# Performance work log

Measured on AMD Instinct MI355X. Metric: run time of the kernel, lower is better.

Reference implementation:

```python
import jax, jax.numpy as jnp
import numpy as np
from jax import lax

SQRT2 = float(np.sqrt(2.0))  # lrelu def_gain
LRELU_SLOPE = 0.2


def setup_inputs() -> dict:
    key = jax.random.key(0)
    ks = jax.random.split(key, 4)
    N, I, O, WD, H = 16, 256, 512, 512, 64
    return {
        "x": jax.random.normal(ks[0], (N, I, H, H), dtype=jnp.float32),
        "w": jax.random.normal(ks[1], (N, WD), dtype=jnp.float32),
        "affine_w": jax.random.normal(ks[2], (I, WD), dtype=jnp.float32),
        "affine_b": jnp.ones((I,), dtype=jnp.float32),
        "weight": jax.random.normal(ks[3], (O, I, 3, 3), dtype=jnp.float32),
        "bias": jnp.zeros((O,), dtype=jnp.float32),
    }


def reference(x, w, affine_w, affine_b, weight, bias):
    N, I, H, W = x.shape
    O, _, kh, kw = weight.shape
    w_dim = affine_w.shape[1]

    # affine (FullyConnectedLayer, weight_gain = 1/sqrt(w_dim))
    styles = w @ (affine_w.T / np.sqrt(w_dim)) + affine_b  # [N, I]

    # modulate + demodulate -> per-sample weights [N, O, I, kh, kw]
    ww = weight[None] * styles[:, None, :, None, None]
    dcoefs = lax.rsqrt(jnp.sum(ww * ww, axis=(2, 3, 4)) + 1e-8)  # [N, O]
    ww = ww * dcoefs[:, :, None, None, None]

    # resample filter: outer([1,3,3,1])/sum, symmetric so flip is a no-op
    f1 = jnp.array([1.0, 3.0, 3.0, 1.0], dtype=x.dtype)
    f1 = f1 / f1.sum()
    f2 = jnp.outer(f1, f1)  # [4, 4]

    # upfirdn2d: pad by padding + (fw-down+1)//2 = 2 per side, depthwise 4x4
    xp = jnp.pad(x, ((0, 0), (0, 0), (2, 2), (2, 2)))
    fk = jnp.broadcast_to(f2[None, None], (I, 1, 4, 4))
    xf = lax.conv_general_dilated(
        xp, fk, window_strides=(1, 1), padding="VALID",
        feature_group_count=I,
        dimension_numbers=("NCHW", "OIHW", "NCHW"))  # [N, I, H+1, W+1]

    # fused grouped conv, stride 2; flip_weight=False -> flip kernel spatially
    wk = ww[:, :, :, ::-1, ::-1].reshape(N * O, I, kh, kw)
    xg = xf.reshape(1, N * I, xf.shape[2], xf.shape[3])
    y = lax.conv_general_dilated(
        xg, wk, window_strides=(2, 2), padding="VALID",
        feature_group_count=N,
        dimension_numbers=("NCHW", "OIHW", "NCHW"))
    y = y.reshape(N, O, y.shape[2], y.shape[3])  # [N, O, H/2, W/2]

    # bias + lrelu, act_gain = sqrt(2), no clamp
    y = y + bias[None, :, None, None]
    y = jnp.where(y >= 0, y, LRELU_SLOPE * y) * SQRT2
    return y
```

## Files before the change

kernel.cpp:

```cpp
#include <hip/hip_runtime.h>
#include <cstdint>
#include <cstddef>


typedef short bf16x8 __attribute__((ext_vector_type(8)));
typedef float f32x4  __attribute__((ext_vector_type(4)));

#define CGSTR 4460544
#define NSTR  278784
#define PLSTR 69696

__device__ __forceinline__ unsigned short f2bf(float f) {
  union { float f; unsigned u; } v; v.f = f;
  unsigned r = (v.u + 0x7FFFu + ((v.u >> 16) & 1u)) >> 16;
  return (unsigned short)r;
}

__device__ __forceinline__ void gload_lds16(const void* g, void* l) {
  __builtin_amdgcn_global_load_lds((const __attribute__((address_space(1))) void*)g,
                                   (__attribute__((address_space(3))) void*)l,
                                   16, 0, 0);
}

__global__ void styles_kernel(const float* __restrict__ w, const float* __restrict__ aw,
                              const float* __restrict__ ab, float* __restrict__ styles) {
  const int n = blockIdx.x;
  const int i = threadIdx.x;
  const float4* wr = (const float4*)(w + (size_t)n * 512);
  const float4* ar = (const float4*)(aw + (size_t)i * 512);
  float acc = 0.f;
#pragma unroll 4
  for (int k = 0; k < 128; ++k) {
    float4 a = wr[k], c = ar[k];
    acc += a.x * c.x + a.y * c.y + a.z * c.z + a.w * c.w;
  }
  styles[n * 256 + i] = acc * 0.04419417382415922f + ab[i];
}

__global__ void wsq_kernel(const float* __restrict__ wt, float* __restrict__ wsq) {
  const int o = blockIdx.x;
  const int i = threadIdx.x;
  const float* p = wt + ((size_t)o * 256 + i) * 9;
  float s = 0.f;
#pragma unroll
  for (int k = 0; k < 9; ++k) s += p[k] * p[k];
  wsq[o * 256 + i] = s;
}

__global__ void dcoefs_kernel(const float* __restrict__ wsq, const float* __restrict__ styles,
                              float* __restrict__ dcoefs) {
  __shared__ float st2[256];
  const int n = blockIdx.x;
  const int t = threadIdx.x;
  if (t < 256) { float s = styles[n * 256 + t]; st2[t] = s * s; }
  __syncthreads();
  const float4* wr = (const float4*)(wsq + (size_t)t * 256);
  const float4* sr = (const float4*)st2;
  float acc = 0.f;
#pragma unroll 4
  for (int k = 0; k < 64; ++k) {
    float4 a = wr[k], c = sr[k];
    acc += a.x * c.x + a.y * c.y + a.z * c.z + a.w * c.w;
  }
  dcoefs[n * 512 + t] = 1.0f / sqrtf(acc + 1e-8f);
}

__global__ void wtcvt_kernel(const float* __restrict__ wt, unsigned short* __restrict__ wtb) {
  const int o = blockIdx.x;
  const int i = threadIdx.x;
  const float* p = wt + ((size_t)o * 256 + i) * 9;
  float v[9];
#pragma unroll
  for (int k = 0; k < 9; ++k) v[k] = p[k];
#pragma unroll
  for (int tap = 0; tap < 9; ++tap)
    wtb[((size_t)tap * 512 + o) * 256 + i] = f2bf(v[8 - tap]);
}

__global__ __launch_bounds__(256, 4) void blur_kernel(const float* __restrict__ x,
                                                      const float* __restrict__ styles,
                                                      unsigned short* __restrict__ xfp) {
  __shared__ float vfls[2][64][71];
  const int b = blockIdx.x;
  const int n = b >> 6;
  const int rem = b & 63;
  const int rg = rem >> 2;
  const int cg = rem & 3;
  const int tid = threadIdx.x;
  const int ch = tid >> 2;
  const int col0 = (tid & 3) * 16;
  const float* xin = x + ((size_t)(n * 256 + cg * 64 + ch) << 12);
  const float s = styles[n * 256 + cg * 64 + ch];
  const float F0s = 0.125f * s, F1s = 0.375f * s;
  const float F0 = 0.125f, F1 = 0.375f;
  const int ybase = rg * 4;
  const int ylim = (rg == 15) ? 5 : 4;
  const size_t obase = (size_t)(cg * 16 + n) * 4 * PLSTR;

  float4 rA[4], rB[4], rC[4], rD[4], rN[4];
  auto load4 = [&](int row, float4* dst) {
    if ((unsigned)row < 64u) {
      const float4* p = (const float4*)(xin + row * 64 + col0);
      dst[0] = p[0]; dst[1] = p[1]; dst[2] = p[2]; dst[3] = p[3];
    } else {
      const float4 z = {0.f, 0.f, 0.f, 0.f};
      dst[0] = z; dst[1] = z; dst[2] = z; dst[3] = z;
    }
  };
  load4(ybase - 2, rA); load4(ybase - 1, rB); load4(ybase, rC); load4(ybase + 1, rD);

  if ((tid & 3) == 0) {
    vfls[0][ch][0] = 0.f; vfls[0][ch][1] = 0.f;
    vfls[1][ch][0] = 0.f; vfls[1][ch][1] = 0.f;
  }
  if ((tid & 3) == 3) {
    vfls[0][ch][66] = 0.f; vfls[0][ch][67] = 0.f; vfls[0][ch][68] = 0.f;
    vfls[1][ch][66] = 0.f; vfls[1][ch][67] = 0.f; vfls[1][ch][68] = 0.f;
  }

#pragma unroll 1
  for (int yy = 0; yy < ylim; ++yy) {
    const int y = ybase + yy;
    load4(y + 2, rN);
    float* vrow = &vfls[yy & 1][ch][2 + col0];
#pragma unroll
    for (int q = 0; q < 4; ++q) {
      vrow[q * 4 + 0] = F0s * rA[q].x + F1s * rB[q].x + F1s * rC[q].x + F0s * rD[q].x;
      vrow[q * 4 + 1] = F0s * rA[q].y + F1s * rB[q].y + F1s * rC[q].y + F0s * rD[q].y;
      vrow[q * 4 + 2] = F0s * rA[q].z + F1s * rB[q].z + F1s * rC[q].z + F0s * rD[q].z;
      vrow[q * 4 + 3] = F0s * rA[q].w + F1s * rB[q].w + F1s * rC[q].w + F0s * rD[q].w;
    }
    __syncthreads();
    const int ph = y & 1, r = y >> 1;
    const float (*vb)[71] = vfls[yy & 1];
#pragma unroll 1
    for (int sI = tid; sI < 520; sI += 256) {
      const int p = sI >> 3, j = sI & 7;
      union { bf16x8 v; unsigned short u[8]; } pk;
#pragma unroll
      for (int k = 0; k < 8; ++k) {
        const float* vp = &vb[j * 8 + k][p];
        pk.u[k] = f2bf(F0 * vp[0] + F1 * vp[1] + F1 * vp[2] + F0 * vp[3]);
      }
      const int pw = p & 1, cc = p >> 1;
      const size_t off = obase + (size_t)(ph * 2 + pw) * PLSTR + (r * 33 + cc) * 64 + j * 8;
      *(bf16x8*)(xfp + off) = pk.v;
    }
#pragma unroll
    for (int q = 0; q < 4; ++q) { rA[q] = rB[q]; rB[q] = rC[q]; rC[q] = rD[q]; rD[q] = rN[q]; }
  }
}

__global__ __launch_bounds__(256) void conv_kernel(
    const unsigned short* __restrict__ wtb,
    const unsigned short* __restrict__ xfp,
    const float* __restrict__ dcoefs,
    const float* __restrict__ bias,
    float* __restrict__ out) {
  __shared__ unsigned short As0[4096], As1[4096];
  __shared__ unsigned short Bs0[4096], Bs1[4096];
  const int idx = blockIdx.x;
  const int pt = idx >> 6;
  const int P = idx & 63;
  const int n = P >> 2;
  const int om = P & 3;
  const int o0 = om << 7;
  const int oh0 = pt << 2;
  const int tid = threadIdx.x;
  const int lane = tid & 63;
  const int wv = tid >> 6;
  const int wm = wv >> 1;
  const int wp = wv & 1;
  const int ml = lane & 15;
  const int kq = lane >> 4;

  f32x4 acc[4][4];
  const f32x4 zz = {0.f, 0.f, 0.f, 0.f};
#pragma unroll
  for (int i = 0; i < 4; ++i)
#pragma unroll
    for (int j = 0; j < 4; ++j) acc[i][j] = zz;

  const int s0 = wv * 128 + lane, s1 = s0 + 64;
  const int r0 = s0 >> 2, g0 = (s0 & 3) * 8;
  const int r1 = s1 >> 2, g1 = (s1 & 3) * 8;
  const int aoff0 = (o0 + r0) * 256 + g0;
  const int aoff1 = (o0 + r1) * 256 + g1;
  const int row0 = oh0 + (r0 >> 5), col0 = r0 & 31;
  const int row1 = oh0 + (r1 >> 5), col1 = r1 & 31;
  const size_t nB = (size_t)n * NSTR;

  auto stage = [&](int kt, unsigned short* As, unsigned short* Bs) {
    const int tap = kt >> 3, kb = kt & 7;
    const int kh = (tap * 11) >> 5;
    const int kw = tap - kh * 3;
    const int ph = kh & 1, dr = kh >> 1;
    const int pw = kw & 1, dc = kw >> 1;
    const unsigned short* At = wtb + tap * 131072 + kb * 32;
    gload_lds16(At + aoff0, As + wv * 1024);
    gload_lds16(At + aoff1, As + wv * 1024 + 512);
    const unsigned short* Bt = xfp + (size_t)(kb >> 1) * CGSTR + nB +
                               (size_t)(ph * 2 + pw) * PLSTR + (kb & 1) * 32;
    gload_lds16(Bt + ((row0 + dr) * 33 + col0 + dc) * 64 + g0, Bs + wv * 1024);
    gload_lds16(Bt + ((row1 + dr) * 33 + col1 + dc) * 64 + g1, Bs + wv * 1024 + 512);
  };
  auto compute = [&](const unsigned short* As, const unsigned short* Bs) {
    bf16x8 af[4], bfv[4];
    const bf16x8* A8 = (const bf16x8*)As;
    const bf16x8* B8 = (const bf16x8*)Bs;
#pragma unroll
    for (int t = 0; t < 4; ++t) {
      af[t]  = A8[(wm * 64 + t * 16 + ml) * 4 + kq];
      bfv[t] = B8[(wp * 64 + t * 16 + ml) * 4 + kq];
    }
#pragma unroll
    for (int mt = 0; mt < 4; ++mt)
#pragma unroll
      for (int nt = 0; nt < 4; ++nt)
        acc[mt][nt] = __builtin_amdgcn_mfma_f32_16x16x32_bf16(af[mt], bfv[nt], acc[mt][nt], 0, 0, 0);
  };

  stage(0, As0, Bs0);
#pragma unroll 1
  for (int kt = 0; kt < 72; kt += 2) {
    __syncthreads();
    stage(kt + 1, As1, Bs1);
    compute(As0, Bs0);
    __syncthreads();
    if (kt + 2 < 72) stage(kt + 2, As0, Bs0);
    compute(As1, Bs1);
  }

  f32x4 dc4[4], bi4[4];
#pragma unroll
  for (int mt = 0; mt < 4; ++mt) {
    const int ob = o0 + wm * 64 + mt * 16 + kq * 4;
    dc4[mt] = *(const f32x4*)(dcoefs + n * 512 + ob);
    bi4[mt] = *(const f32x4*)(bias + ob);
  }
#pragma unroll
  for (int mt = 0; mt < 4; ++mt) {
#pragma unroll
    for (int nt = 0; nt < 4; ++nt) {
      const int p = wp * 64 + nt * 16 + ml;
      const int oh = oh0 + (p >> 5), ow = p & 31;
#pragma unroll
      for (int r = 0; r < 4; ++r) {
        const int o = o0 + wm * 64 + mt * 16 + kq * 4 + r;
        float v = acc[mt][nt][r] * dc4[mt][r] + bi4[mt][r];
        v = (v >= 0.f ? v : 0.2f * v) * 1.41421356237309515f;
        out[(((size_t)n * 512 + o) * 32 + oh) * 32 + ow] = v;
      }
    }
  }
}

extern "C" void kernel_launch(void* const* d_in, const int* in_sizes, int n_in,
                              void* d_out, int out_size, void* d_ws, size_t ws_size,
                              hipStream_t stream) {
  const float* x  = (const float*)d_in[0];
  const float* w  = (const float*)d_in[1];
  const float* aw = (const float*)d_in[2];
  const float* ab = (const float*)d_in[3];
  const float* wt = (const float*)d_in[4];
  const float* bs = (const float*)d_in[5];
  float* out = (float*)d_out;

  char* ws = (char*)d_ws;
  float* styles        = (float*)(ws);
  float* dcoefs        = (float*)(ws + 16384);
  float* wsq           = (float*)(ws + 49152);
  unsigned short* wtb  = (unsigned short*)(ws + 573440);
  unsigned short* xfp  = (unsigned short*)(ws + 2932736);

  styles_kernel<<<dim3(16),   dim3(256), 0, stream>>>(w, aw, ab, styles);
  wsq_kernel   <<<dim3(512),  dim3(256), 0, stream>>>(wt, wsq);
  dcoefs_kernel<<<dim3(16),   dim3(512), 0, stream>>>(wsq, styles, dcoefs);
  wtcvt_kernel <<<dim3(512),  dim3(256), 0, stream>>>(wt, wtb);
  blur_kernel  <<<dim3(1024), dim3(256), 0, stream>>>(x, styles, xfp);
  conv_kernel  <<<dim3(512),  dim3(256), 0, stream>>>(wtb, xfp, dcoefs, bs, out);
}
```

Before: 221.0 us.

## Fuse weight prep kernels, do horizontal blur in registers, remap conv blocks

```diff
diff --git a/kernel.cpp b/kernel.cpp
--- a/kernel.cpp
+++ b/kernel.cpp
@@ -37,14 +37,19 @@
   styles[n * 256 + i] = acc * 0.04419417382415922f + ab[i];
 }
 
-__global__ void wsq_kernel(const float* __restrict__ wt, float* __restrict__ wsq) {
+__global__ void wtcvt_kernel(const float* __restrict__ wt, unsigned short* __restrict__ wtb,
+                             float* __restrict__ wsq) {
   const int o = blockIdx.x;
   const int i = threadIdx.x;
   const float* p = wt + ((size_t)o * 256 + i) * 9;
+  float v[9];
   float s = 0.f;
 #pragma unroll
-  for (int k = 0; k < 9; ++k) s += p[k] * p[k];
+  for (int k = 0; k < 9; ++k) { v[k] = p[k]; s += v[k] * v[k]; }
   wsq[o * 256 + i] = s;
+#pragma unroll
+  for (int tap = 0; tap < 9; ++tap)
+    wtb[((size_t)tap * 512 + o) * 256 + i] = f2bf(v[8 - tap]);
 }
 
 __global__ void dcoefs_kernel(const float* __restrict__ wsq, const float* __restrict__ styles,
@@ -65,22 +70,10 @@
   dcoefs[n * 512 + t] = 1.0f / sqrtf(acc + 1e-8f);
 }
 
-__global__ void wtcvt_kernel(const float* __restrict__ wt, unsigned short* __restrict__ wtb) {
-  const int o = blockIdx.x;
-  const int i = threadIdx.x;
-  const float* p = wt + ((size_t)o * 256 + i) * 9;
-  float v[9];
-#pragma unroll
-  for (int k = 0; k < 9; ++k) v[k] = p[k];
-#pragma unroll
-  for (int tap = 0; tap < 9; ++tap)
-    wtb[((size_t)tap * 512 + o) * 256 + i] = f2bf(v[8 - tap]);
-}
-
 __global__ __launch_bounds__(256, 4) void blur_kernel(const float* __restrict__ x,
                                                       const float* __restrict__ styles,
                                                       unsigned short* __restrict__ xfp) {
-  __shared__ float vfls[2][64][71];
+  __shared__ unsigned short shls[2][64][68];
   const int b = blockIdx.x;
   const int n = b >> 6;
   const int rem = b & 63;
@@ -88,10 +81,11 @@
   const int cg = rem & 3;
   const int tid = threadIdx.x;
   const int ch = tid >> 2;
-  const int col0 = (tid & 3) * 16;
+  const int s4 = tid & 3;
+  const int col0 = s4 * 16;
   const float* xin = x + ((size_t)(n * 256 + cg * 64 + ch) << 12);
-  const float s = styles[n * 256 + cg * 64 + ch];
-  const float F0s = 0.125f * s, F1s = 0.375f * s;
+  const float sv = styles[n * 256 + cg * 64 + ch];
+  const float F0s = 0.125f * sv, F1s = 0.375f * sv;
   const float F0 = 0.125f, F1 = 0.375f;
   const int ybase = rg * 4;
   const int ylim = (rg == 15) ? 5 : 4;
@@ -109,42 +103,45 @@
   };
   load4(ybase - 2, rA); load4(ybase - 1, rB); load4(ybase, rC); load4(ybase + 1, rD);
 
-  if ((tid & 3) == 0) {
-    vfls[0][ch][0] = 0.f; vfls[0][ch][1] = 0.f;
-    vfls[1][ch][0] = 0.f; vfls[1][ch][1] = 0.f;
-  }
-  if ((tid & 3) == 3) {
-    vfls[0][ch][66] = 0.f; vfls[0][ch][67] = 0.f; vfls[0][ch][68] = 0.f;
-    vfls[1][ch][66] = 0.f; vfls[1][ch][67] = 0.f; vfls[1][ch][68] = 0.f;
-  }
-
 #pragma unroll 1
   for (int yy = 0; yy < ylim; ++yy) {
     const int y = ybase + yy;
     load4(y + 2, rN);
-    float* vrow = &vfls[yy & 1][ch][2 + col0];
+    float ve[20];
 #pragma unroll
     for (int q = 0; q < 4; ++q) {
-      vrow[q * 4 + 0] = F0s * rA[q].x + F1s * rB[q].x + F1s * rC[q].x + F0s * rD[q].x;
-      vrow[q * 4 + 1] = F0s * rA[q].y + F1s * rB[q].y + F1s * rC[q].y + F0s * rD[q].y;
-      vrow[q * 4 + 2] = F0s * rA[q].z + F1s * rB[q].z + F1s * rC[q].z + F0s * rD[q].z;
-      vrow[q * 4 + 3] = F0s * rA[q].w + F1s * rB[q].w + F1s * rC[q].w + F0s * rD[q].w;
-    }
+      ve[2 + q * 4 + 0] = F0s * rA[q].x + F1s * rB[q].x + F1s * rC[q].x + F0s * rD[q].x;
+      ve[2 + q * 4 + 1] = F0s * rA[q].y + F1s * rB[q].y + F1s * rC[q].y + F0s * rD[q].y;
+      ve[2 + q * 4 + 2] = F0s * rA[q].z + F1s * rB[q].z + F1s * rC[q].z + F0s * rD[q].z;
+      ve[2 + q * 4 + 3] = F0s * rA[q].w + F1s * rB[q].w + F1s * rC[q].w + F0s * rD[q].w;
+    }
+    float vm2 = __shfl_up(ve[16], 1);
+    float vm1 = __shfl_up(ve[17], 1);
+    float vp1 = __shfl_down(ve[2], 1);
+    if (s4 == 0) { vm2 = 0.f; vm1 = 0.f; }
+    if (s4 == 3) vp1 = 0.f;
+    ve[0] = vm2; ve[1] = vm1; ve[18] = vp1; ve[19] = 0.f;
+    unsigned short hv[17];
+#pragma unroll
+    for (int pl = 0; pl < 17; ++pl)
+      hv[pl] = f2bf(F0 * ve[pl] + F1 * ve[pl + 1] + F1 * ve[pl + 2] + F0 * ve[pl + 3]);
+    unsigned short (*sh)[68] = shls[yy & 1];
+    unsigned* dst32 = (unsigned*)&sh[ch][col0];
+#pragma unroll
+    for (int q = 0; q < 8; ++q)
+      dst32[q] = (unsigned)hv[2 * q] | ((unsigned)hv[2 * q + 1] << 16);
+    if (s4 == 3) sh[ch][64] = hv[16];
     __syncthreads();
     const int ph = y & 1, r = y >> 1;
-    const float (*vb)[71] = vfls[yy & 1];
 #pragma unroll 1
     for (int sI = tid; sI < 520; sI += 256) {
       const int p = sI >> 3, j = sI & 7;
-      union { bf16x8 v; unsigned short u[8]; } pk;
-#pragma unroll
-      for (int k = 0; k < 8; ++k) {
-        const float* vp = &vb[j * 8 + k][p];
-        pk.u[k] = f2bf(F0 * vp[0] + F1 * vp[1] + F1 * vp[2] + F0 * vp[3]);
-      }
+      union { bf16x8 vv; unsigned short u[8]; } pk;
+#pragma unroll
+      for (int k = 0; k < 8; ++k) pk.u[k] = sh[j * 8 + k][p];
       const int pw = p & 1, cc = p >> 1;
       const size_t off = obase + (size_t)(ph * 2 + pw) * PLSTR + (r * 33 + cc) * 64 + j * 8;
-      *(bf16x8*)(xfp + off) = pk.v;
+      *(bf16x8*)(xfp + off) = pk.vv;
     }
 #pragma unroll
     for (int q = 0; q < 4; ++q) { rA[q] = rB[q]; rB[q] = rC[q]; rC[q] = rD[q]; rD[q] = rN[q]; }
@@ -160,10 +157,10 @@
   __shared__ unsigned short As0[4096], As1[4096];
   __shared__ unsigned short Bs0[4096], Bs1[4096];
   const int idx = blockIdx.x;
-  const int pt = idx >> 6;
-  const int P = idx & 63;
-  const int n = P >> 2;
-  const int om = P & 3;
+  const int om = idx >> 7;
+  const int g = idx & 127;
+  const int pt = g >> 4;
+  const int n = g & 15;
   const int o0 = om << 7;
   const int oh0 = pt << 2;
   const int tid = threadIdx.x;
@@ -274,9 +271,8 @@
   unsigned short* xfp  = (unsigned short*)(ws + 2932736);
 
   styles_kernel<<<dim3(16),   dim3(256), 0, stream>>>(w, aw, ab, styles);
-  wsq_kernel   <<<dim3(512),  dim3(256), 0, stream>>>(wt, wsq);
+  wtcvt_kernel <<<dim3(512),  dim3(256), 0, stream>>>(wt, wtb, wsq);
   dcoefs_kernel<<<dim3(16),   dim3(512), 0, stream>>>(wsq, styles, dcoefs);
-  wtcvt_kernel <<<dim3(512),  dim3(256), 0, stream>>>(wt, wtb);
   blur_kernel  <<<dim3(1024), dim3(256), 0, stream>>>(x, styles, xfp);
   conv_kernel  <<<dim3(512),  dim3(256), 0, stream>>>(wtb, xfp, dcoefs, bs, out);
 }
```

Result: faster. 211.2 us (-4.4%).
